# Kernel tuning notes

Hardware: AMD Instinct MI355X
Metric: run time of the kernel (lower is better)

Reference implementation:

```python
import jax, jax.numpy as jnp
import numpy as np
import math

B, S, D, H, F = 2, 2048, 1024, 16, 4096
HD = D // H  # head size 64
EPS = 1e-5


def layernorm(x, g, b):
    mu = jnp.mean(x, axis=-1, keepdims=True)
    var = jnp.mean((x - mu) ** 2, axis=-1, keepdims=True)
    return (x - mu) * jax.lax.rsqrt(var + EPS) * g + b


def new_gelu(x):
    c = math.sqrt(2.0 / math.pi)
    return 0.5 * x * (1.0 + jnp.tanh(c * (x + 0.044715 * x ** 3)))


def setup_inputs() -> dict:
    key = jax.random.key(0)
    ks = jax.random.split(key, 20)
    sc = 0.02
    return {
        "x": jax.random.normal(ks[0], (B, S, D), jnp.float32),
        # per-head q/k/v weights stacked: [H, HD, D] (torch Linear weight layout [out,in])
        "Wq": jax.random.normal(ks[1], (H, HD, D), jnp.float32) * sc,
        "bq": jax.random.normal(ks[2], (H, HD), jnp.float32) * sc,
        "Wk": jax.random.normal(ks[3], (H, HD, D), jnp.float32) * sc,
        "bk": jax.random.normal(ks[4], (H, HD), jnp.float32) * sc,
        "Wv": jax.random.normal(ks[5], (H, HD, D), jnp.float32) * sc,
        "bv": jax.random.normal(ks[6], (H, HD), jnp.float32) * sc,
        "Wo": jax.random.normal(ks[7], (D, D), jnp.float32) * sc,
        "bo": jax.random.normal(ks[8], (D,), jnp.float32) * sc,
        "ln1_g": 1.0 + jax.random.normal(ks[9], (D,), jnp.float32) * sc,
        "ln1_b": jax.random.normal(ks[10], (D,), jnp.float32) * sc,
        "W1": jax.random.normal(ks[11], (F, D), jnp.float32) * sc,
        "b1": jax.random.normal(ks[12], (F,), jnp.float32) * sc,
        "W2": jax.random.normal(ks[13], (D, F), jnp.float32) * sc,
        "b2": jax.random.normal(ks[14], (D,), jnp.float32) * sc,
        "ln2_g": 1.0 + jax.random.normal(ks[15], (D,), jnp.float32) * sc,
        "ln2_b": jax.random.normal(ks[16], (D,), jnp.float32) * sc,
    }


def reference(x, Wq, bq, Wk, bk, Wv, bv, Wo, bo, ln1_g, ln1_b, W1, b1, W2, b2, ln2_g, ln2_b):
    # --- pre-LN multi-head attention (dropout is identity in eval) ---
    h = layernorm(x, ln1_g, ln1_b)
    q = jnp.einsum("bsd,hed->bshe", h, Wq) + bq  # [B,S,H,HD]
    k = jnp.einsum("bsd,hed->bshe", h, Wk) + bk
    v = jnp.einsum("bsd,hed->bshe", h, Wv) + bv
    scores = jnp.einsum("bshe,bthe->bhst", q, k) / math.sqrt(HD)
    probs = jax.nn.softmax(scores, axis=-1)
    attn = jnp.einsum("bhst,bthe->bshe", probs, v).reshape(B, S, D)  # concat heads
    attn = attn @ Wo.T + bo
    x = x + attn
    # --- pre-LN MLP with NewGELU ---
    h2 = layernorm(x, ln2_g, ln2_b)
    mlp = new_gelu(h2 @ W1.T + b1) @ W2.T + b2
    return x + mlp
```

## Files before the change

### kernel.cpp

```cpp
#include <hip/hip_runtime.h>

typedef unsigned short u16;
typedef __attribute__((ext_vector_type(8))) __bf16 bf16x8;
typedef __attribute__((ext_vector_type(4))) __bf16 bf16x4;
typedef __attribute__((ext_vector_type(4))) float f32x4;
typedef __attribute__((ext_vector_type(4))) unsigned short u16x4;

#define AS1 __attribute__((address_space(1)))
#define AS3 __attribute__((address_space(3)))

__device__ __forceinline__ void async_load16(const void* g, void* l) {
  __builtin_amdgcn_global_load_lds((const AS1 void*)g, (AS3 void*)l, 16, 0, 0);
}

__device__ __forceinline__ float exp2_fast(float x) {
#if __has_builtin(__builtin_amdgcn_exp2f)
  return __builtin_amdgcn_exp2f(x);
#else
  return exp2f(x);
#endif
}
__device__ __forceinline__ float rcp_fast(float x) {
#if __has_builtin(__builtin_amdgcn_rcpf)
  return __builtin_amdgcn_rcpf(x);
#else
  return 1.0f / x;
#endif
}

__device__ __forceinline__ u16 f2bf(float f) {
  union { float f; unsigned u; } a; a.f = f;
  unsigned u = a.u;
  u += 0x7fffu + ((u >> 16) & 1u);
  return (u16)(u >> 16);
}
__device__ __forceinline__ u16 bf_bits(float f) {
  union { __bf16 b; u16 u; } c; c.b = (__bf16)f; return c.u;
}
__device__ __forceinline__ float bf2f(u16 h) {
  union { unsigned u; float f; } c; c.u = ((unsigned)h) << 16; return c.f;
}

__global__ __launch_bounds__(256)
void f2b_all(const float* __restrict__ s0, const float* __restrict__ s1,
             const float* __restrict__ s2, const float* __restrict__ s3,
             const float* __restrict__ s4, const float* __restrict__ s5,
             u16* __restrict__ dst) {
  const int i = blockIdx.x * 256 + threadIdx.x;
  const float* s; int off;
  if (i < 1048576) {
    if (i < 262144)      { s = s0; off = i; }
    else if (i < 524288) { s = s1; off = i - 262144; }
    else if (i < 786432) { s = s2; off = i - 524288; }
    else                 { s = s3; off = i - 786432; }
  } else if (i < 2097152) { s = s4; off = i - 1048576; }
  else                    { s = s5; off = i - 2097152; }
  const float4 v = ((const float4*)s)[off];
  u16x4 o; o[0] = f2bf(v.x); o[1] = f2bf(v.y); o[2] = f2bf(v.z); o[3] = f2bf(v.w);
  ((u16x4*)dst)[i] = o;
}

__global__ __launch_bounds__(256)
void ln_kernel(const float* __restrict__ x, const float* __restrict__ g,
               const float* __restrict__ b, u16* __restrict__ out) {
  const int row = blockIdx.x, tid = threadIdx.x;
  const float4 v = ((const float4*)(x + (size_t)row * 1024))[tid];
  float s = v.x + v.y + v.z + v.w;
  float s2 = v.x * v.x + v.y * v.y + v.z * v.z + v.w * v.w;
#pragma unroll
  for (int o = 1; o < 64; o <<= 1) { s += __shfl_xor(s, o); s2 += __shfl_xor(s2, o); }
  __shared__ float red[8];
  const int wave = tid >> 6, lane = tid & 63;
  if (lane == 0) { red[wave] = s; red[wave + 4] = s2; }
  __syncthreads();
  s = red[0] + red[1] + red[2] + red[3];
  s2 = red[4] + red[5] + red[6] + red[7];
  const float mu = s * (1.f / 1024.f);
  const float rstd = rsqrtf(s2 * (1.f / 1024.f) - mu * mu + 1e-5f);
  const float4 gg = ((const float4*)g)[tid];
  const float4 bb = ((const float4*)b)[tid];
  u16x4 o4;
  o4[0] = f2bf((v.x - mu) * rstd * gg.x + bb.x);
  o4[1] = f2bf((v.y - mu) * rstd * gg.y + bb.y);
  o4[2] = f2bf((v.z - mu) * rstd * gg.z + bb.z);
  o4[3] = f2bf((v.w - mu) * rstd * gg.w + bb.w);
  ((u16x4*)(out + (size_t)row * 1024))[tid] = o4;
}

__global__ __launch_bounds__(256)
void ln_fuse(const float* __restrict__ x, const u16* __restrict__ parts,
             const float* __restrict__ bo, const float* __restrict__ g,
             const float* __restrict__ b, float* __restrict__ out,
             u16* __restrict__ hb) {
  const int row = blockIdx.x, tid = threadIdx.x;
  const size_t base = (size_t)row * 1024;
  const int i4 = row * 256 + tid;
  const float4 xv = ((const float4*)(x + base))[tid];
  const u16x4 h0 = ((const u16x4*)parts)[i4];
  const u16x4 h1 = ((const u16x4*)(parts + 4194304))[i4];
  const float4 bv = ((const float4*)bo)[tid];
  float4 t;
  t.x = xv.x + bf2f(h0[0]) + bf2f(h1[0]) + bv.x;
  t.y = xv.y + bf2f(h0[1]) + bf2f(h1[1]) + bv.y;
  t.z = xv.z + bf2f(h0[2]) + bf2f(h1[2]) + bv.z;
  t.w = xv.w + bf2f(h0[3]) + bf2f(h1[3]) + bv.w;
  ((float4*)(out + base))[tid] = t;
  float s = t.x + t.y + t.z + t.w;
  float s2 = t.x * t.x + t.y * t.y + t.z * t.z + t.w * t.w;
#pragma unroll
  for (int o = 1; o < 64; o <<= 1) { s += __shfl_xor(s, o); s2 += __shfl_xor(s2, o); }
  __shared__ float red[8];
  const int wave = tid >> 6, lane = tid & 63;
  if (lane == 0) { red[wave] = s; red[wave + 4] = s2; }
  __syncthreads();
  s = red[0] + red[1] + red[2] + red[3];
  s2 = red[4] + red[5] + red[6] + red[7];
  const float mu = s * (1.f / 1024.f);
  const float rstd = rsqrtf(s2 * (1.f / 1024.f) - mu * mu + 1e-5f);
  const float4 gg = ((const float4*)g)[tid];
  const float4 bb = ((const float4*)b)[tid];
  u16x4 o4;
  o4[0] = f2bf((t.x - mu) * rstd * gg.x + bb.x);
  o4[1] = f2bf((t.y - mu) * rstd * gg.y + bb.y);
  o4[2] = f2bf((t.z - mu) * rstd * gg.z + bb.z);
  o4[3] = f2bf((t.w - mu) * rstd * gg.w + bb.w);
  ((u16x4*)(hb + base))[tid] = o4;
}

__global__ __launch_bounds__(256)
void add4(float* __restrict__ out, const u16* __restrict__ p,
          const float* __restrict__ b2) {
  const int i = blockIdx.x * 256 + threadIdx.x;
  const float4 o = ((const float4*)out)[i];
  const float4 bv = ((const float4*)b2)[i & 255];
  float a0 = o.x + bv.x, a1 = o.y + bv.y, a2 = o.z + bv.z, a3 = o.w + bv.w;
#pragma unroll
  for (int kz = 0; kz < 4; kz++) {
    const u16x4 h = ((const u16x4*)(p + (size_t)kz * 4194304))[i];
    a0 += bf2f(h[0]); a1 += bf2f(h[1]); a2 += bf2f(h[2]); a3 += bf2f(h[3]);
  }
  float4 r; r.x = a0; r.y = a1; r.z = a2; r.w = a3;
  ((float4*)out)[i] = r;
}

template <class Epi>
__global__ __launch_bounds__(256, 2)
void gemm_bt(const u16* __restrict__ A, const u16* __restrict__ Bw,
             int ldk, int K, int NB, Epi epi) {
  __shared__ __align__(16) u16 As[256 * 64];
  __shared__ __align__(16) u16 Bs[128 * 64];
  const int tid = threadIdx.x;
  const int wave = tid >> 6, lane = tid & 63;
  const int quad = lane >> 4, l16 = lane & 15;
  const int id = blockIdx.x;
  const int mb = id & 15;
  const int t = id >> 4;
  const int nb = t % NB;
  const int kz = t / NB;
  const int bm = mb * 256, bn = nb * 128;
  const int wm = wave * 64;

  const int srow = lane >> 3;
  const int chunk = lane & 7;
  const int scol = ((chunk ^ srow) * 8);
  const u16* pa[8];
  u16* la[8];
#pragma unroll
  for (int j = 0; j < 8; j++) {
    pa[j] = A + (size_t)(bm + wave * 64 + j * 8 + srow) * ldk + (size_t)kz * K + scol;
    la[j] = &As[wave * 4096 + j * 512];
  }
  const u16* pb[4];
  u16* lb[4];
#pragma unroll
  for (int j = 0; j < 4; j++) {
    pb[j] = Bw + (size_t)(bn + wave * 32 + j * 8 + srow) * ldk + (size_t)kz * K + scol;
    lb[j] = &Bs[wave * 2048 + j * 512];
  }

  const f32x4 fz = {0.f, 0.f, 0.f, 0.f};
  f32x4 acc[4][8];
#pragma unroll
  for (int i = 0; i < 4; i++)
#pragma unroll
    for (int j = 0; j < 8; j++) acc[i][j] = fz;

  const int key = (l16 & 7);

  for (int k0 = 0; k0 < K; k0 += 64) {
#pragma unroll
    for (int j = 0; j < 8; j++) { async_load16(pa[j], la[j]); pa[j] += 64; }
#pragma unroll
    for (int j = 0; j < 4; j++) { async_load16(pb[j], lb[j]); pb[j] += 64; }
    __syncthreads();
#pragma unroll
    for (int kk = 0; kk < 2; kk++) {
      const int slot = ((kk * 4 + quad) ^ key) * 8;
      bf16x8 af[4], bfr[8];
#pragma unroll
      for (int mi = 0; mi < 4; mi++)
        af[mi] = *(const bf16x8*)&As[(wm + mi * 16 + l16) * 64 + slot];
#pragma unroll
      for (int ni = 0; ni < 8; ni++)
        bfr[ni] = *(const bf16x8*)&Bs[(ni * 16 + l16) * 64 + slot];
#pragma unroll
      for (int mi = 0; mi < 4; mi++)
#pragma unroll
        for (int ni = 0; ni < 8; ni++)
          acc[mi][ni] = __builtin_amdgcn_mfma_f32_16x16x32_bf16(af[mi], bfr[ni], acc[mi][ni], 0, 0, 0);
    }
    __syncthreads();
  }
#pragma unroll
  for (int mi = 0; mi < 4; mi++)
#pragma unroll
    for (int ni = 0; ni < 8; ni++)
      epi(bm + wm + mi * 16 + quad * 4, bn + ni * 16 + l16, kz, acc[mi][ni]);
}

struct EpiQKV {
  u16 *q, *k, *vt; const float *bq, *bk, *bv;
  __device__ void operator()(int m0, int n, int, f32x4 v) const {
    const int which = n >> 10, nn = n & 1023;
    const int hh = nn >> 6, e = nn & 63;
    const int bb = m0 >> 11, s0 = m0 & 2047;
    const size_t bh = (size_t)(bb * 16 + hh);
    if (which == 0) {
      const float bias = bq[nn];
      u16* p = &q[(bh * 2048 + s0) * 64 + e];
#pragma unroll
      for (int r = 0; r < 4; r++) p[r * 64] = bf_bits((v[r] + bias) * 0.18033688f);
    } else if (which == 1) {
      const float bias = bk[nn];
      u16* p = &k[(bh * 2048 + s0) * 64 + e];
#pragma unroll
      for (int r = 0; r < 4; r++) p[r * 64] = bf_bits(v[r] + bias);
    } else {
      const float bias = bv[nn];
      bf16x4 pk;
#pragma unroll
      for (int r = 0; r < 4; r++) pk[r] = (__bf16)(v[r] + bias);
      *(bf16x4*)&vt[(bh * 64 + e) * 2048 + s0] = pk;
    }
  }
};
struct EpiPartB {
  u16* p;
  __device__ void operator()(int m0, int n, int kz, f32x4 v) const {
    u16* pp = p + (size_t)kz * 4194304;
#pragma unroll
    for (int r = 0; r < 4; r++) pp[(size_t)(m0 + r) * 1024 + n] = bf_bits(v[r]);
  }
};
struct EpiGelu {
  const float* b1; u16* o;
  __device__ void operator()(int m0, int n, int, f32x4 v) const {
    const float bias = b1[n];
#pragma unroll
    for (int r = 0; r < 4; r++) {
      const float u = v[r] + bias;
      const float z2 = u * (2.3021183f + 0.10294515f * u * u);
      const float d = 1.0f + exp2_fast(-z2);
      o[(size_t)(m0 + r) * 4096 + n] = bf_bits(u * rcp_fast(d));
    }
  }
};

__global__ __launch_bounds__(256)
void attn_kernel(const u16* __restrict__ Q, const u16* __restrict__ K,
                 const u16* __restrict__ Vt, u16* __restrict__ O) {
  __shared__ __align__(16) u16 Ks[64 * 72];
  __shared__ __align__(16) u16 Vs[64 * 72];
  __shared__ __align__(16) u16 Ps[4][32 * 72];
  const int tid = threadIdx.x, wave = tid >> 6, lane = tid & 63;
  const int quad = lane >> 4, l16 = lane & 15;
  const int b = blockIdx.z, h = blockIdx.y, qt = blockIdx.x;
  const size_t bh = (size_t)(b * 16 + h);
  const u16* Qp = Q + bh * (size_t)(2048 * 64);
  const u16* Kp = K + bh * (size_t)(2048 * 64);
  const u16* Vp = Vt + bh * (size_t)(64 * 2048);
  const int q0 = qt * 128 + wave * 32;

  bf16x8 qf[2][2];
#pragma unroll
  for (int rg = 0; rg < 2; rg++) {
    const u16* qrow = &Qp[(size_t)(q0 + rg * 16 + l16) * 64 + quad * 8];
    qf[rg][0] = *(const bf16x8*)qrow;
    qf[rg][1] = *(const bf16x8*)(qrow + 32);
  }

  const int sr = tid >> 2, sc = (tid & 3) * 16;
  const int krow = 4 * (sr & 15) + (sr >> 4);
  const u16* kg = &Kp[(size_t)krow * 64 + sc];
  const u16* vg = &Vp[(size_t)sr * 2048 + sc];
  u16* kl = &Ks[sr * 72 + sc];
  u16* vl = &Vs[sr * 72 + sc];
  u16* Pw = &Ps[wave][0];

  bf16x8 ones;
#pragma unroll
  for (int i = 0; i < 8; i++) ones[i] = (__bf16)1.0f;

  const f32x4 fz = {0.f, 0.f, 0.f, 0.f};
  f32x4 acc[2][4], lsum[2];
#pragma unroll
  for (int rg = 0; rg < 2; rg++) {
    lsum[rg] = fz;
#pragma unroll
    for (int g = 0; g < 4; g++) acc[rg][g] = fz;
  }

  bf16x8 pk0 = *(const bf16x8*)kg, pk1 = *(const bf16x8*)(kg + 8);
  bf16x8 pv0 = *(const bf16x8*)vg, pv1 = *(const bf16x8*)(vg + 8);

  for (int t0 = 0; t0 < 2048; t0 += 64) {
    *(bf16x8*)kl = pk0; *(bf16x8*)(kl + 8) = pk1;
    *(bf16x8*)vl = pv0; *(bf16x8*)(vl + 8) = pv1;
    __syncthreads();
    kg += 64 * 64; vg += 64;
    pk0 = *(const bf16x8*)kg; pk1 = *(const bf16x8*)(kg + 8);
    pv0 = *(const bf16x8*)vg; pv1 = *(const bf16x8*)(vg + 8);

    f32x4 s[2][4];
    __builtin_amdgcn_s_setprio(1);
#pragma unroll
    for (int g = 0; g < 4; g++) {
      const u16* kr = &Ks[(g * 16 + l16) * 72 + quad * 8];
      const bf16x8 kb0 = *(const bf16x8*)kr;
      const bf16x8 kb1 = *(const bf16x8*)(kr + 32);
#pragma unroll
      for (int rg = 0; rg < 2; rg++) {
        f32x4 z = __builtin_amdgcn_mfma_f32_16x16x32_bf16(qf[rg][0], kb0, fz, 0, 0, 0);
        s[rg][g] = __builtin_amdgcn_mfma_f32_16x16x32_bf16(qf[rg][1], kb1, z, 0, 0, 0);
      }
    }
    __builtin_amdgcn_s_setprio(0);
#pragma unroll
    for (int rg = 0; rg < 2; rg++)
#pragma unroll
      for (int r = 0; r < 4; r++) {
        f32x4 pf;
#pragma unroll
        for (int g = 0; g < 4; g++) pf[g] = exp2_fast(s[rg][g][r]);
        const bf16x4 pb = __builtin_convertvector(pf, bf16x4);
        *(bf16x4*)&Pw[(rg * 16 + quad * 4 + r) * 72 + 4 * l16] = pb;
      }
    bf16x8 pa[2][2];
#pragma unroll
    for (int rg = 0; rg < 2; rg++) {
      const u16* pr = &Pw[(rg * 16 + l16) * 72 + quad * 8];
      pa[rg][0] = *(const bf16x8*)pr;
      pa[rg][1] = *(const bf16x8*)(pr + 32);
      lsum[rg] = __builtin_amdgcn_mfma_f32_16x16x32_bf16(pa[rg][0], ones, lsum[rg], 0, 0, 0);
      lsum[rg] = __builtin_amdgcn_mfma_f32_16x16x32_bf16(pa[rg][1], ones, lsum[rg], 0, 0, 0);
    }
    __builtin_amdgcn_s_setprio(1);
#pragma unroll
    for (int g = 0; g < 4; g++) {
      const u16* vr = &Vs[(g * 16 + l16) * 72 + quad * 8];
      const bf16x8 vb0 = *(const bf16x8*)vr;
      const bf16x8 vb1 = *(const bf16x8*)(vr + 32);
#pragma unroll
      for (int rg = 0; rg < 2; rg++) {
        acc[rg][g] = __builtin_amdgcn_mfma_f32_16x16x32_bf16(pa[rg][0], vb0, acc[rg][g], 0, 0, 0);
        acc[rg][g] = __builtin_amdgcn_mfma_f32_16x16x32_bf16(pa[rg][1], vb1, acc[rg][g], 0, 0, 0);
      }
    }
    __builtin_amdgcn_s_setprio(0);
    __syncthreads();
  }
#pragma unroll
  for (int rg = 0; rg < 2; rg++)
#pragma unroll
    for (int r = 0; r < 4; r++) {
      const float inv = rcp_fast(lsum[rg][r]);
      const int s_row = q0 + rg * 16 + quad * 4 + r;
      u16* op = (u16*)&O[((size_t)(b * 2048 + s_row)) * 1024 + h * 64 + l16];
#pragma unroll
      for (int g = 0; g < 4; g++) op[g * 16] = bf_bits(acc[rg][g][r] * inv);
    }
}

extern "C" void kernel_launch(void* const* d_in, const int* in_sizes, int n_in,
                              void* d_out, int out_size, void* d_ws, size_t ws_size,
                              hipStream_t stream) {
  const float* x   = (const float*)d_in[0];
  const float* Wq  = (const float*)d_in[1];
  const float* bq  = (const float*)d_in[2];
  const float* Wk  = (const float*)d_in[3];
  const float* bk  = (const float*)d_in[4];
  const float* Wv  = (const float*)d_in[5];
  const float* bv  = (const float*)d_in[6];
  const float* Wo  = (const float*)d_in[7];
  const float* bo  = (const float*)d_in[8];
  const float* g1  = (const float*)d_in[9];
  const float* be1 = (const float*)d_in[10];
  const float* W1  = (const float*)d_in[11];
  const float* b1  = (const float*)d_in[12];
  const float* W2  = (const float*)d_in[13];
  const float* b2  = (const float*)d_in[14];
  const float* g2  = (const float*)d_in[15];
  const float* be2 = (const float*)d_in[16];
  float* out = (float*)d_out;

  char* w = (char*)d_ws;
  u16* wqkv = (u16*)w; w += (size_t)3072 * 1024 * 2;
  u16* wob  = (u16*)w; w += (size_t)1024 * 1024 * 2;
  u16* w1b  = (u16*)w; w += (size_t)4096 * 1024 * 2;
  u16* w2b  = (u16*)w; w += (size_t)1024 * 4096 * 2;
  u16* hb   = (u16*)w; w += (size_t)4096 * 1024 * 2;
  u16* qb   = (u16*)w; w += (size_t)4096 * 1024 * 2;
  u16* kb   = (u16*)w; w += (size_t)4096 * 1024 * 2;
  u16* vtb  = (u16*)w; w += (size_t)4096 * 1024 * 2;
  u16* atb  = (u16*)w; w += (size_t)4096 * 1024 * 2;
  u16* m1b  = (u16*)w; w += (size_t)4096 * 4096 * 2;

  u16* op_part = m1b;
  u16* ml_part = qb;

  f2b_all<<<12288, 256, 0, stream>>>(Wq, Wk, Wv, Wo, W1, W2, wqkv);

  ln_kernel<<<4096, 256, 0, stream>>>(x, g1, be1, hb);
  gemm_bt<EpiQKV><<<384, 256, 0, stream>>>(hb, wqkv, 1024, 1024, 24,
      EpiQKV{qb, kb, vtb, bq, bk, bv});
  attn_kernel<<<dim3(16, 16, 2), 256, 0, stream>>>(qb, kb, vtb, atb);
  gemm_bt<EpiPartB><<<256, 256, 0, stream>>>(atb, wob, 1024, 512, 8,
      EpiPartB{op_part});
  ln_fuse<<<4096, 256, 0, stream>>>(x, op_part, bo, g2, be2, out, hb);
  gemm_bt<EpiGelu><<<512, 256, 0, stream>>>(hb, w1b, 1024, 1024, 32,
      EpiGelu{b1, m1b});
  gemm_bt<EpiPartB><<<512, 256, 0, stream>>>(m1b, w2b, 4096, 1024, 8,
      EpiPartB{ml_part});
  add4<<<4096, 256, 0, stream>>>(out, ml_part, b2);
}
```

Baseline: 341.0 us.

## Double attention KV tile to 128 keys and simplify GEMM LDS swizzle

The attention kernel now processes 128 keys per iteration instead of 64. It computes two score halves and writes them interleaved into a wider P buffer so that P·V runs over a K=128 chunk. This halves the number of block barriers and global prefetch rounds per head, at the cost of more LDS and more registers for the prefetch buffers. Separately, the GEMM LDS XOR swizzle is replaced by a simpler pattern that flips only the bit-2 row group, which changes the bank-conflict behavior of the fragment reads.

```diff
diff --git a/kernel.cpp b/kernel.cpp
--- a/kernel.cpp
+++ b/kernel.cpp
@@ -162,7 +162,7 @@
 
   const int srow = lane >> 3;
   const int chunk = lane & 7;
-  const int scol = ((chunk ^ srow) * 8);
+  const int scol = (chunk ^ (2 * ((srow >> 2) & 1))) * 8;
   const u16* pa[8];
   u16* la[8];
 #pragma unroll
@@ -185,7 +185,7 @@
 #pragma unroll
     for (int j = 0; j < 8; j++) acc[i][j] = fz;
 
-  const int key = (l16 & 7);
+  const int qsw = (quad ^ (2 * ((l16 >> 2) & 1))) * 8;
 
   for (int k0 = 0; k0 < K; k0 += 64) {
 #pragma unroll
@@ -195,7 +195,7 @@
     __syncthreads();
 #pragma unroll
     for (int kk = 0; kk < 2; kk++) {
-      const int slot = ((kk * 4 + quad) ^ key) * 8;
+      const int slot = qsw + kk * 32;
       bf16x8 af[4], bfr[8];
 #pragma unroll
       for (int mi = 0; mi < 4; mi++)
@@ -269,9 +269,9 @@
 __global__ __launch_bounds__(256)
 void attn_kernel(const u16* __restrict__ Q, const u16* __restrict__ K,
                  const u16* __restrict__ Vt, u16* __restrict__ O) {
-  __shared__ __align__(16) u16 Ks[64 * 72];
-  __shared__ __align__(16) u16 Vs[64 * 72];
-  __shared__ __align__(16) u16 Ps[4][32 * 72];
+  __shared__ __align__(16) u16 Ks[128 * 72];
+  __shared__ __align__(16) u16 Vs[64 * 136];
+  __shared__ __align__(16) u16 Ps[4][32 * 136];
   const int tid = threadIdx.x, wave = tid >> 6, lane = tid & 63;
   const int quad = lane >> 4, l16 = lane & 15;
   const int b = blockIdx.z, h = blockIdx.y, qt = blockIdx.x;
@@ -289,12 +289,13 @@
     qf[rg][1] = *(const bf16x8*)(qrow + 32);
   }
 
-  const int sr = tid >> 2, sc = (tid & 3) * 16;
-  const int krow = 4 * (sr & 15) + (sr >> 4);
-  const u16* kg = &Kp[(size_t)krow * 64 + sc];
-  const u16* vg = &Vp[(size_t)sr * 2048 + sc];
-  u16* kl = &Ks[sr * 72 + sc];
-  u16* vl = &Vs[sr * 72 + sc];
+  const int srK = tid >> 1, scK = (tid & 1) * 32;
+  const int krow = 8 * (srK & 15) + (srK >> 4);
+  const u16* kg = &Kp[(size_t)krow * 64 + scK];
+  u16* kl = &Ks[srK * 72 + scK];
+  const int srV = tid >> 2, scV = (tid & 3) * 32;
+  const u16* vg = &Vp[(size_t)srV * 2048 + scV];
+  u16* vl = &Vs[srV * 136 + scV];
   u16* Pw = &Ps[wave][0];
 
   bf16x8 ones;
@@ -310,16 +311,26 @@
     for (int g = 0; g < 4; g++) acc[rg][g] = fz;
   }
 
-  bf16x8 pk0 = *(const bf16x8*)kg, pk1 = *(const bf16x8*)(kg + 8);
-  bf16x8 pv0 = *(const bf16x8*)vg, pv1 = *(const bf16x8*)(vg + 8);
-
-  for (int t0 = 0; t0 < 2048; t0 += 64) {
-    *(bf16x8*)kl = pk0; *(bf16x8*)(kl + 8) = pk1;
-    *(bf16x8*)vl = pv0; *(bf16x8*)(vl + 8) = pv1;
+  bf16x8 pk[4], pv[4];
+#pragma unroll
+  for (int c = 0; c < 4; c++) {
+    pk[c] = *(const bf16x8*)(kg + 8 * c);
+    pv[c] = *(const bf16x8*)(vg + 8 * c);
+  }
+
+  for (int t0 = 0; t0 < 2048; t0 += 128) {
+#pragma unroll
+    for (int c = 0; c < 4; c++) {
+      *(bf16x8*)(kl + 8 * c) = pk[c];
+      *(bf16x8*)(vl + 8 * c) = pv[c];
+    }
     __syncthreads();
-    kg += 64 * 64; vg += 64;
-    pk0 = *(const bf16x8*)kg; pk1 = *(const bf16x8*)(kg + 8);
-    pv0 = *(const bf16x8*)vg; pv1 = *(const bf16x8*)(vg + 8);
+    kg += 128 * 64; vg += 128;
+#pragma unroll
+    for (int c = 0; c < 4; c++) {
+      pk[c] = *(const bf16x8*)(kg + 8 * c);
+      pv[c] = *(const bf16x8*)(vg + 8 * c);
+    }
 
     f32x4 s[2][4];
     __builtin_amdgcn_s_setprio(1);
@@ -343,27 +354,50 @@
 #pragma unroll
         for (int g = 0; g < 4; g++) pf[g] = exp2_fast(s[rg][g][r]);
         const bf16x4 pb = __builtin_convertvector(pf, bf16x4);
-        *(bf16x4*)&Pw[(rg * 16 + quad * 4 + r) * 72 + 4 * l16] = pb;
-      }
-    bf16x8 pa[2][2];
-#pragma unroll
-    for (int rg = 0; rg < 2; rg++) {
-      const u16* pr = &Pw[(rg * 16 + l16) * 72 + quad * 8];
-      pa[rg][0] = *(const bf16x8*)pr;
-      pa[rg][1] = *(const bf16x8*)(pr + 32);
-      lsum[rg] = __builtin_amdgcn_mfma_f32_16x16x32_bf16(pa[rg][0], ones, lsum[rg], 0, 0, 0);
-      lsum[rg] = __builtin_amdgcn_mfma_f32_16x16x32_bf16(pa[rg][1], ones, lsum[rg], 0, 0, 0);
-    }
+        *(bf16x4*)&Pw[(rg * 16 + quad * 4 + r) * 136 + 8 * l16] = pb;
+      }
     __builtin_amdgcn_s_setprio(1);
 #pragma unroll
     for (int g = 0; g < 4; g++) {
-      const u16* vr = &Vs[(g * 16 + l16) * 72 + quad * 8];
-      const bf16x8 vb0 = *(const bf16x8*)vr;
-      const bf16x8 vb1 = *(const bf16x8*)(vr + 32);
+      const u16* kr = &Ks[((g + 4) * 16 + l16) * 72 + quad * 8];
+      const bf16x8 kb0 = *(const bf16x8*)kr;
+      const bf16x8 kb1 = *(const bf16x8*)(kr + 32);
 #pragma unroll
       for (int rg = 0; rg < 2; rg++) {
-        acc[rg][g] = __builtin_amdgcn_mfma_f32_16x16x32_bf16(pa[rg][0], vb0, acc[rg][g], 0, 0, 0);
-        acc[rg][g] = __builtin_amdgcn_mfma_f32_16x16x32_bf16(pa[rg][1], vb1, acc[rg][g], 0, 0, 0);
+        f32x4 z = __builtin_amdgcn_mfma_f32_16x16x32_bf16(qf[rg][0], kb0, fz, 0, 0, 0);
+        s[rg][g] = __builtin_amdgcn_mfma_f32_16x16x32_bf16(qf[rg][1], kb1, z, 0, 0, 0);
+      }
+    }
+    __builtin_amdgcn_s_setprio(0);
+#pragma unroll
+    for (int rg = 0; rg < 2; rg++)
+#pragma unroll
+      for (int r = 0; r < 4; r++) {
+        f32x4 pf;
+#pragma unroll
+        for (int g = 0; g < 4; g++) pf[g] = exp2_fast(s[rg][g][r]);
+        const bf16x4 pb = __builtin_convertvector(pf, bf16x4);
+        *(bf16x4*)&Pw[(rg * 16 + quad * 4 + r) * 136 + 8 * l16 + 4] = pb;
+      }
+
+    bf16x8 pa[2][4];
+#pragma unroll
+    for (int rg = 0; rg < 2; rg++)
+#pragma unroll
+      for (int hh2 = 0; hh2 < 4; hh2++) {
+        pa[rg][hh2] = *(const bf16x8*)&Pw[(rg * 16 + l16) * 136 + quad * 8 + hh2 * 32];
+        lsum[rg] = __builtin_amdgcn_mfma_f32_16x16x32_bf16(pa[rg][hh2], ones, lsum[rg], 0, 0, 0);
+      }
+    __builtin_amdgcn_s_setprio(1);
+#pragma unroll
+    for (int g = 0; g < 4; g++) {
+      const u16* vr = &Vs[(g * 16 + l16) * 136 + quad * 8];
+#pragma unroll
+      for (int hh2 = 0; hh2 < 4; hh2++) {
+        const bf16x8 vb = *(const bf16x8*)(vr + hh2 * 32);
+#pragma unroll
+        for (int rg = 0; rg < 2; rg++)
+          acc[rg][g] = __builtin_amdgcn_mfma_f32_16x16x32_bf16(pa[rg][hh2], vb, acc[rg][g], 0, 0, 0);
       }
     }
     __builtin_amdgcn_s_setprio(0);
```

Result: faster. 333.9 us (-2.1%).

## Split attention over key halves with combine kernel; split-K 4 for out-proj; new LDS swizzle

Applied to the files above, without the earlier changes.

The attention kernel now splits the key/value sequence in two, doubling the grid. Each half writes unnormalized fp32 partial outputs and row sums, and a new combine kernel merges them into the bf16 attention output. This is meant to raise occupancy, since the previous grid had only 512 blocks. The output-projection GEMM moves from split-K 2 to split-K 4, and ln_fuse sums four partials. The GEMM LDS swizzle also changes to a simpler XOR pattern. The cost is extra fp32 partial traffic, one more launch, and possibly more bank conflicts from the new swizzle.

```diff
diff --git a/kernel.cpp b/kernel.cpp
--- a/kernel.cpp
+++ b/kernel.cpp
@@ -96,14 +96,14 @@
   const size_t base = (size_t)row * 1024;
   const int i4 = row * 256 + tid;
   const float4 xv = ((const float4*)(x + base))[tid];
-  const u16x4 h0 = ((const u16x4*)parts)[i4];
-  const u16x4 h1 = ((const u16x4*)(parts + 4194304))[i4];
   const float4 bv = ((const float4*)bo)[tid];
   float4 t;
-  t.x = xv.x + bf2f(h0[0]) + bf2f(h1[0]) + bv.x;
-  t.y = xv.y + bf2f(h0[1]) + bf2f(h1[1]) + bv.y;
-  t.z = xv.z + bf2f(h0[2]) + bf2f(h1[2]) + bv.z;
-  t.w = xv.w + bf2f(h0[3]) + bf2f(h1[3]) + bv.w;
+  t.x = xv.x + bv.x; t.y = xv.y + bv.y; t.z = xv.z + bv.z; t.w = xv.w + bv.w;
+#pragma unroll
+  for (int kz = 0; kz < 4; kz++) {
+    const u16x4 h = ((const u16x4*)(parts + (size_t)kz * 4194304))[i4];
+    t.x += bf2f(h[0]); t.y += bf2f(h[1]); t.z += bf2f(h[2]); t.w += bf2f(h[3]);
+  }
   ((float4*)(out + base))[tid] = t;
   float s = t.x + t.y + t.z + t.w;
   float s2 = t.x * t.x + t.y * t.y + t.z * t.z + t.w * t.w;
@@ -162,7 +162,7 @@
 
   const int srow = lane >> 3;
   const int chunk = lane & 7;
-  const int scol = ((chunk ^ srow) * 8);
+  const int scol = (chunk ^ (2 * ((srow >> 2) & 1))) * 8;
   const u16* pa[8];
   u16* la[8];
 #pragma unroll
@@ -185,7 +185,7 @@
 #pragma unroll
     for (int j = 0; j < 8; j++) acc[i][j] = fz;
 
-  const int key = (l16 & 7);
+  const int qsw = (quad ^ (2 * ((l16 >> 2) & 1))) * 8;
 
   for (int k0 = 0; k0 < K; k0 += 64) {
 #pragma unroll
@@ -195,7 +195,7 @@
     __syncthreads();
 #pragma unroll
     for (int kk = 0; kk < 2; kk++) {
-      const int slot = ((kk * 4 + quad) ^ key) * 8;
+      const int slot = qsw + kk * 32;
       bf16x8 af[4], bfr[8];
 #pragma unroll
       for (int mi = 0; mi < 4; mi++)
@@ -268,17 +268,19 @@
 
 __global__ __launch_bounds__(256)
 void attn_kernel(const u16* __restrict__ Q, const u16* __restrict__ K,
-                 const u16* __restrict__ Vt, u16* __restrict__ O) {
+                 const u16* __restrict__ Vt, float* __restrict__ part,
+                 float* __restrict__ lsums) {
   __shared__ __align__(16) u16 Ks[64 * 72];
   __shared__ __align__(16) u16 Vs[64 * 72];
   __shared__ __align__(16) u16 Ps[4][32 * 72];
   const int tid = threadIdx.x, wave = tid >> 6, lane = tid & 63;
   const int quad = lane >> 4, l16 = lane & 15;
-  const int b = blockIdx.z, h = blockIdx.y, qt = blockIdx.x;
-  const size_t bh = (size_t)(b * 16 + h);
-  const u16* Qp = Q + bh * (size_t)(2048 * 64);
-  const u16* Kp = K + bh * (size_t)(2048 * 64);
-  const u16* Vp = Vt + bh * (size_t)(64 * 2048);
+  const int z = blockIdx.z, h = blockIdx.y, qt = blockIdx.x;
+  const int b = z >> 1, sp = z & 1;
+  const int bh = b * 16 + h;
+  const u16* Qp = Q + (size_t)bh * (2048 * 64);
+  const u16* Kp = K + (size_t)bh * (2048 * 64) + (size_t)sp * (1024 * 64);
+  const u16* Vp = Vt + (size_t)bh * (64 * 2048) + (size_t)sp * 1024;
   const int q0 = qt * 128 + wave * 32;
 
   bf16x8 qf[2][2];
@@ -313,11 +315,12 @@
   bf16x8 pk0 = *(const bf16x8*)kg, pk1 = *(const bf16x8*)(kg + 8);
   bf16x8 pv0 = *(const bf16x8*)vg, pv1 = *(const bf16x8*)(vg + 8);
 
-  for (int t0 = 0; t0 < 2048; t0 += 64) {
+  for (int t0 = 0; t0 < 1024; t0 += 64) {
     *(bf16x8*)kl = pk0; *(bf16x8*)(kl + 8) = pk1;
     *(bf16x8*)vl = pv0; *(bf16x8*)(vl + 8) = pv1;
     __syncthreads();
-    kg += 64 * 64; vg += 64;
+    const int adv = (t0 + 64 < 1024) ? 64 : 0;
+    kg += adv * 64; vg += adv;
     pk0 = *(const bf16x8*)kg; pk1 = *(const bf16x8*)(kg + 8);
     pv0 = *(const bf16x8*)vg; pv1 = *(const bf16x8*)(vg + 8);
 
@@ -330,8 +333,8 @@
       const bf16x8 kb1 = *(const bf16x8*)(kr + 32);
 #pragma unroll
       for (int rg = 0; rg < 2; rg++) {
-        f32x4 z = __builtin_amdgcn_mfma_f32_16x16x32_bf16(qf[rg][0], kb0, fz, 0, 0, 0);
-        s[rg][g] = __builtin_amdgcn_mfma_f32_16x16x32_bf16(qf[rg][1], kb1, z, 0, 0, 0);
+        f32x4 z2 = __builtin_amdgcn_mfma_f32_16x16x32_bf16(qf[rg][0], kb0, fz, 0, 0, 0);
+        s[rg][g] = __builtin_amdgcn_mfma_f32_16x16x32_bf16(qf[rg][1], kb1, z2, 0, 0, 0);
       }
     }
     __builtin_amdgcn_s_setprio(0);
@@ -369,16 +372,35 @@
     __builtin_amdgcn_s_setprio(0);
     __syncthreads();
   }
+  float* pp = part + (size_t)(sp * 32 + bh) * 131072;
 #pragma unroll
   for (int rg = 0; rg < 2; rg++)
 #pragma unroll
     for (int r = 0; r < 4; r++) {
-      const float inv = rcp_fast(lsum[rg][r]);
       const int s_row = q0 + rg * 16 + quad * 4 + r;
-      u16* op = (u16*)&O[((size_t)(b * 2048 + s_row)) * 1024 + h * 64 + l16];
-#pragma unroll
-      for (int g = 0; g < 4; g++) op[g * 16] = bf_bits(acc[rg][g][r] * inv);
-    }
+      float* op = pp + (size_t)s_row * 64 + l16;
+#pragma unroll
+      for (int g = 0; g < 4; g++) op[g * 16] = acc[rg][g][r];
+      if (l16 == 0)
+        lsums[(size_t)(sp * 32 + bh) * 2048 + s_row] = lsum[rg][r];
+    }
+}
+
+__global__ __launch_bounds__(256)
+void attn_combine(const float* __restrict__ part, const float* __restrict__ lsums,
+                  u16* __restrict__ O) {
+  const int i = blockIdx.x * 256 + threadIdx.x;
+  const int bh = i >> 15, rem = i & 32767;
+  const int s = rem >> 4, eg = rem & 15;
+  const f32x4 a0 = ((const f32x4*)part)[(size_t)bh * 32768 + rem];
+  const f32x4 a1 = ((const f32x4*)part)[(size_t)(32 + bh) * 32768 + rem];
+  const float l = lsums[(size_t)bh * 2048 + s] + lsums[(size_t)(32 + bh) * 2048 + s];
+  const float inv = rcp_fast(l);
+  bf16x4 o;
+#pragma unroll
+  for (int c = 0; c < 4; c++) o[c] = (__bf16)((a0[c] + a1[c]) * inv);
+  const int b = bh >> 4, h = bh & 15;
+  *(bf16x4*)&O[((size_t)(b * 2048 + s)) * 1024 + h * 64 + eg * 4] = o;
 }
 
 extern "C" void kernel_launch(void* const* d_in, const int* in_sizes, int n_in,
@@ -417,14 +439,17 @@
 
   u16* op_part = m1b;
   u16* ml_part = qb;
+  float* apart = (float*)m1b;
+  float* alsum = (float*)hb;
 
   f2b_all<<<12288, 256, 0, stream>>>(Wq, Wk, Wv, Wo, W1, W2, wqkv);
 
   ln_kernel<<<4096, 256, 0, stream>>>(x, g1, be1, hb);
   gemm_bt<EpiQKV><<<384, 256, 0, stream>>>(hb, wqkv, 1024, 1024, 24,
       EpiQKV{qb, kb, vtb, bq, bk, bv});
-  attn_kernel<<<dim3(16, 16, 2), 256, 0, stream>>>(qb, kb, vtb, atb);
-  gemm_bt<EpiPartB><<<256, 256, 0, stream>>>(atb, wob, 1024, 512, 8,
+  attn_kernel<<<dim3(16, 16, 4), 256, 0, stream>>>(qb, kb, vtb, apart, alsum);
+  attn_combine<<<4096, 256, 0, stream>>>(apart, alsum, atb);
+  gemm_bt<EpiPartB><<<512, 256, 0, stream>>>(atb, wob, 1024, 256, 8,
       EpiPartB{op_part});
   ln_fuse<<<4096, 256, 0, stream>>>(x, op_part, bo, g2, be2, out, hb);
   gemm_bt<EpiGelu><<<512, 256, 0, stream>>>(hb, w1b, 1024, 1024, 32,
```

Measured after the change: 341.1 us. About the same (+0.0%).
